# Performance work log

Hardware: AMD Instinct MI355X
Metric: run time of the kernel (lower is better)

The kernel has to match this reference:

```python
import jax, jax.numpy as jnp
import numpy as np

B, L, Z, H = 8, 256, 16, 256


def setup_inputs() -> dict:
    key = jax.random.key(0)
    k1, k2, k3, k4 = jax.random.split(key, 4)
    start_logits = jax.random.normal(k1, (B, L, H), dtype=jnp.float32)
    end_logits = jax.random.normal(k2, (B, L, H), dtype=jnp.float32)
    cls_logits = jax.random.normal(k3, (B, Z, H), dtype=jnp.float32)
    # nn.init.normal_(std=0.1)
    weight_start_end = 0.1 * jax.random.normal(k4, (H, H, H), dtype=jnp.float32)
    return {
        "start_logits": start_logits,
        "end_logits": end_logits,
        "cls_logits": cls_logits,
        "weight_start_end": weight_start_end,
    }


def reference(start_logits, end_logits, cls_logits, weight_start_end):
    # start: [b,x,i], weight: [i,o,j], end: [b,y,j], cls: [b,z,o]
    # Stage 1a: contract i ->  [b,x,o,j]  (GEMM: (b*x, i) @ (i, o*j))
    sw = jnp.einsum('bxi,ioj->bxoj', start_logits, weight_start_end)
    # Stage 1b: contract j ->  [b,x,y,o]
    start_end = jnp.einsum('bxoj,byj->bxyo', sw, end_logits)
    # Stage 2: contract o ->  [b,x,y,z]
    span_logits = jnp.einsum('bxyo,bzo->bxyz', start_end, cls_logits)
    return span_logits
```

## Files before the change

### kernel.cpp

```cpp
#include <hip/hip_runtime.h>
#include <hip/hip_bf16.h>


typedef __attribute__((ext_vector_type(8))) short      bf16x8;
typedef __attribute__((ext_vector_type(8))) unsigned short u16x8;
typedef __attribute__((ext_vector_type(4))) float      f32x4;

#define LDST 40

__device__ __forceinline__ unsigned short f2bf(float f) {
    unsigned u = __builtin_bit_cast(unsigned, f);
    u += 0x7fff + ((u >> 16) & 1);
    return (unsigned short)(u >> 16);
}

template<bool AB16, bool BB16, bool BTRANS, bool CB16>
__global__ __launch_bounds__(256)
void gemm_mfma(const void* __restrict__ Abv, const void* __restrict__ Bbv,
               void* __restrict__ Cbv,
               int lda, int ldb, int ldc,
               long aBS, int aSh, long bBS, int bSh, long cBS)
{
    __shared__ unsigned short As[128 * LDST];
    __shared__ unsigned short Bs[128 * LDST];

    const int tid  = threadIdx.x;
    const int bz   = blockIdx.z;
    const int row0 = blockIdx.y * 128;
    const int col0 = blockIdx.x * 128;

    const float*          Af = (const float*)Abv          + (long)(bz >> aSh) * aBS;
    const unsigned short* Ah = (const unsigned short*)Abv + (long)(bz >> aSh) * aBS;
    const float*          Bf = (const float*)Bbv          + (long)(bz >> bSh) * bBS;
    const unsigned short* Bh = (const unsigned short*)Bbv + (long)(bz >> bSh) * bBS;
    float*          Cf = (float*)Cbv          + (long)bz * cBS;
    unsigned short* Ch = (unsigned short*)Cbv + (long)bz * cBS;

    const int ar  = tid >> 2;
    const int akc = tid & 3;
    const int bk2 = (tid & 15) * 2;
    const int bn0 = (tid >> 4) * 8;

    const int wid = tid >> 6, lane = tid & 63;
    const int wm = wid >> 1, wn = wid & 1;
    const int lr = lane & 15, lg = lane >> 4;

    f32x4 acc[4][4] = {};

    float4 aPf[2][2]; u16x8 aPh[2];
    float4 bNf[2][2]; u16x8 bNh[2];
    float4 bTf[4];    u16x8 bTh[2];

    auto LOAD = [&](int k0) {
#pragma unroll
        for (int it = 0; it < 2; ++it) {
            if constexpr (!AB16) {
                const float* p = Af + (long)(row0 + ar + 64 * it) * lda + k0 + akc * 8;
                aPf[it][0] = *(const float4*)p;
                aPf[it][1] = *(const float4*)(p + 4);
            } else {
                aPh[it] = *(const u16x8*)(Ah + (long)(row0 + ar + 64 * it) * lda + k0 + akc * 8);
            }
            if constexpr (!BTRANS) {
                if constexpr (!BB16) {
                    const float* p = Bf + (long)(col0 + ar + 64 * it) * ldb + k0 + akc * 8;
                    bNf[it][0] = *(const float4*)p;
                    bNf[it][1] = *(const float4*)(p + 4);
                } else {
                    bNh[it] = *(const u16x8*)(Bh + (long)(col0 + ar + 64 * it) * ldb + k0 + akc * 8);
                }
            }
        }
        if constexpr (BTRANS) {
            if constexpr (!BB16) {
                const float* p = Bf + (long)(k0 + bk2) * ldb + col0 + bn0;
                bTf[0] = *(const float4*)p;
                bTf[1] = *(const float4*)(p + 4);
                bTf[2] = *(const float4*)(p + ldb);
                bTf[3] = *(const float4*)(p + ldb + 4);
            } else {
                const unsigned short* p = Bh + (long)(k0 + bk2) * ldb + col0 + bn0;
                bTh[0] = *(const u16x8*)p;
                bTh[1] = *(const u16x8*)(p + ldb);
            }
        }
    };

    auto WRITE = [&]() {
#pragma unroll
        for (int it = 0; it < 2; ++it) {
            u16x8 w;
            if constexpr (!AB16) {
                const float* v = (const float*)&aPf[it][0];
#pragma unroll
                for (int e = 0; e < 8; ++e) w[e] = f2bf(v[e]);
            } else {
                w = aPh[it];
            }
            *(u16x8*)(As + (ar + 64 * it) * LDST + akc * 8) = w;

            if constexpr (!BTRANS) {
                u16x8 wb;
                if constexpr (!BB16) {
                    const float* v = (const float*)&bNf[it][0];
#pragma unroll
                    for (int e = 0; e < 8; ++e) wb[e] = f2bf(v[e]);
                } else {
                    wb = bNh[it];
                }
                *(u16x8*)(Bs + (ar + 64 * it) * LDST + akc * 8) = wb;
            }
        }
        if constexpr (BTRANS) {
#pragma unroll
            for (int e = 0; e < 8; ++e) {
                unsigned lo, hi;
                if constexpr (!BB16) {
                    const float* v0 = (const float*)&bTf[0];
                    const float* v1 = (const float*)&bTf[2];
                    lo = f2bf(v0[e]); hi = f2bf(v1[e]);
                } else {
                    lo = bTh[0][e]; hi = bTh[1][e];
                }
                *(unsigned*)(Bs + (bn0 + e) * LDST + bk2) = lo | (hi << 16);
            }
        }
    };

    auto COMPUTE = [&]() {
        bf16x8 aF[4], bF[4];
#pragma unroll
        for (int f = 0; f < 4; ++f) {
            aF[f] = *(const bf16x8*)&As[(wm * 64 + f * 16 + lr) * LDST + lg * 8];
            bF[f] = *(const bf16x8*)&Bs[(wn * 64 + f * 16 + lr) * LDST + lg * 8];
        }
#pragma unroll
        for (int fm = 0; fm < 4; ++fm)
#pragma unroll
            for (int fn = 0; fn < 4; ++fn)
                acc[fm][fn] = __builtin_amdgcn_mfma_f32_16x16x32_bf16(
                    aF[fm], bF[fn], acc[fm][fn], 0, 0, 0);
    };

    LOAD(0);
#pragma unroll
    for (int s = 0; s < 8; ++s) {
        WRITE();
        if (s < 7) LOAD((s + 1) * 32);
        __syncthreads();
        COMPUTE();
        __syncthreads();
    }

#pragma unroll
    for (int fm = 0; fm < 4; ++fm)
#pragma unroll
        for (int q = 0; q < 4; ++q) {
            const long row = row0 + wm * 64 + fm * 16 + lg * 4 + q;
#pragma unroll
            for (int fn = 0; fn < 4; ++fn) {
                const int col = col0 + wn * 64 + fn * 16 + lr;
                if constexpr (CB16) Ch[row * ldc + col] = f2bf(acc[fm][fn][q]);
                else                Cf[row * ldc + col] = acc[fm][fn][q];
            }
        }
}

__global__ __launch_bounds__(256)
void ztranspose(const float* __restrict__ tmp, float* __restrict__ out)
{
    __shared__ float lds[256][17];
    const int tid = threadIdx.x;
    const int b = blockIdx.x >> 8;
    const int x = blockIdx.x & 255;

#pragma unroll
    for (int z = 0; z < 16; ++z)
        lds[tid][z] = tmp[((long)(b * 16 + z) * 256 + x) * 256 + tid];
    __syncthreads();

    float* op = out + (long)(b * 256 + x) * 4096;
#pragma unroll
    for (int q = 0; q < 4; ++q) {
        const int y  = q * 64 + (tid >> 2);
        const int z0 = (tid & 3) * 4;
        float4 v = { lds[y][z0], lds[y][z0 + 1], lds[y][z0 + 2], lds[y][z0 + 3] };
        *(float4*)(op + (q * 256 + tid) * 4) = v;
    }
}

extern "C" void kernel_launch(void* const* d_in, const int* in_sizes, int n_in,
                              void* d_out, int out_size, void* d_ws, size_t ws_size,
                              hipStream_t stream)
{
    const float* start = (const float*)d_in[0];
    const float* endl  = (const float*)d_in[1];
    const float* cls   = (const float*)d_in[2];
    const float* W     = (const float*)d_in[3];
    float* out = (float*)d_out;

    unsigned short* Wc  = (unsigned short*)d_ws;
    unsigned short* T   = (unsigned short*)d_out;
    float*          tmp = (float*)d_ws;

    hipLaunchKernelGGL((gemm_mfma<false, false, true, true>), dim3(2, 1, 256), dim3(256), 0, stream,
        (const void*)cls, (const void*)W, (void*)Wc,
        256, 256, 65536, 0L, 0, 65536L, 0, 256L);

    hipLaunchKernelGGL((gemm_mfma<false, true, true, true>), dim3(2, 2, 128), dim3(256), 0, stream,
        (const void*)start, (const void*)Wc, (void*)T,
        256, 256, 256, 65536L, 4, 65536L, 0, 65536L);

    hipLaunchKernelGGL((gemm_mfma<true, false, false, false>), dim3(2, 2, 128), dim3(256), 0, stream,
        (const void*)T, (const void*)endl, (void*)tmp,
        256, 256, 256, 65536L, 0, 65536L, 4, 65536L);

    hipLaunchKernelGGL(ztranspose, dim3(2048), dim3(256), 0, stream, tmp, out);
}
```

Baseline: 157.3 us.

## Double-buffer LDS tiles, use 512-thread blocks, and vectorize transpose loads

The GEMM kernel moves to 512 threads per block, so each wave computes a 32x64 sub-tile. LDS tiles are now double-buffered, which drops one barrier per k-step and lets global-to-LDS writes for the next stage overlap the MFMA work on the current buffer. MFMA sections are raised in priority with s_setprio. The z-transpose kernel now reads float4 vectors instead of scalars. The trade-off is more LDS per block and a hand-written waitcnt/barrier sequence that has to stay correct for the buffer reuse.

```diff
diff --git a/kernel.cpp b/kernel.cpp
--- a/kernel.cpp
+++ b/kernel.cpp
@@ -1,10 +1,10 @@
 #include <hip/hip_runtime.h>
-#include <hip/hip_bf16.h>
-
-
-typedef __attribute__((ext_vector_type(8))) short      bf16x8;
+
+
+typedef __attribute__((ext_vector_type(8))) short          bf16x8;
 typedef __attribute__((ext_vector_type(8))) unsigned short u16x8;
-typedef __attribute__((ext_vector_type(4))) float      f32x4;
+typedef __attribute__((ext_vector_type(4))) unsigned short u16x4;
+typedef __attribute__((ext_vector_type(4))) float          f32x4;
 
 #define LDST 40
 
@@ -15,14 +15,14 @@
 }
 
 template<bool AB16, bool BB16, bool BTRANS, bool CB16>
-__global__ __launch_bounds__(256)
+__global__ __launch_bounds__(512, 4)
 void gemm_mfma(const void* __restrict__ Abv, const void* __restrict__ Bbv,
                void* __restrict__ Cbv,
                int lda, int ldb, int ldc,
                long aBS, int aSh, long bBS, int bSh, long cBS)
 {
-    __shared__ unsigned short As[128 * LDST];
-    __shared__ unsigned short Bs[128 * LDST];
+    __shared__ unsigned short As[2][128 * LDST];
+    __shared__ unsigned short Bs[2][128 * LDST];
 
     const int tid  = threadIdx.x;
     const int bz   = blockIdx.z;
@@ -38,125 +38,119 @@
 
     const int ar  = tid >> 2;
     const int akc = tid & 3;
-    const int bk2 = (tid & 15) * 2;
-    const int bn0 = (tid >> 4) * 8;
+    const int kp  = (tid >> 5) * 2;
+    const int ng  = (tid & 31) * 4;
 
     const int wid = tid >> 6, lane = tid & 63;
     const int wm = wid >> 1, wn = wid & 1;
     const int lr = lane & 15, lg = lane >> 4;
 
-    f32x4 acc[4][4] = {};
-
-    float4 aPf[2][2]; u16x8 aPh[2];
-    float4 bNf[2][2]; u16x8 bNh[2];
-    float4 bTf[4];    u16x8 bTh[2];
+    f32x4 acc[2][4] = {};
+
+    float4 aPf[2]; u16x8 aPh;
+    float4 bNf[2]; u16x8 bNh;
+    float4 bTf[2]; u16x4 bTh[2];
 
     auto LOAD = [&](int k0) {
-#pragma unroll
-        for (int it = 0; it < 2; ++it) {
-            if constexpr (!AB16) {
-                const float* p = Af + (long)(row0 + ar + 64 * it) * lda + k0 + akc * 8;
-                aPf[it][0] = *(const float4*)p;
-                aPf[it][1] = *(const float4*)(p + 4);
+        if constexpr (!AB16) {
+            const float* p = Af + (long)(row0 + ar) * lda + k0 + akc * 8;
+            aPf[0] = *(const float4*)p;
+            aPf[1] = *(const float4*)(p + 4);
+        } else {
+            aPh = *(const u16x8*)(Ah + (long)(row0 + ar) * lda + k0 + akc * 8);
+        }
+        if constexpr (!BTRANS) {
+            if constexpr (!BB16) {
+                const float* p = Bf + (long)(col0 + ar) * ldb + k0 + akc * 8;
+                bNf[0] = *(const float4*)p;
+                bNf[1] = *(const float4*)(p + 4);
             } else {
-                aPh[it] = *(const u16x8*)(Ah + (long)(row0 + ar + 64 * it) * lda + k0 + akc * 8);
-            }
-            if constexpr (!BTRANS) {
-                if constexpr (!BB16) {
-                    const float* p = Bf + (long)(col0 + ar + 64 * it) * ldb + k0 + akc * 8;
-                    bNf[it][0] = *(const float4*)p;
-                    bNf[it][1] = *(const float4*)(p + 4);
-                } else {
-                    bNh[it] = *(const u16x8*)(Bh + (long)(col0 + ar + 64 * it) * ldb + k0 + akc * 8);
-                }
-            }
-        }
-        if constexpr (BTRANS) {
+                bNh = *(const u16x8*)(Bh + (long)(col0 + ar) * ldb + k0 + akc * 8);
+            }
+        } else {
             if constexpr (!BB16) {
-                const float* p = Bf + (long)(k0 + bk2) * ldb + col0 + bn0;
+                const float* p = Bf + (long)(k0 + kp) * ldb + col0 + ng;
                 bTf[0] = *(const float4*)p;
-                bTf[1] = *(const float4*)(p + 4);
-                bTf[2] = *(const float4*)(p + ldb);
-                bTf[3] = *(const float4*)(p + ldb + 4);
+                bTf[1] = *(const float4*)(p + ldb);
             } else {
-                const unsigned short* p = Bh + (long)(k0 + bk2) * ldb + col0 + bn0;
-                bTh[0] = *(const u16x8*)p;
-                bTh[1] = *(const u16x8*)(p + ldb);
+                const unsigned short* p = Bh + (long)(k0 + kp) * ldb + col0 + ng;
+                bTh[0] = *(const u16x4*)p;
+                bTh[1] = *(const u16x4*)(p + ldb);
             }
         }
     };
 
-    auto WRITE = [&]() {
-#pragma unroll
-        for (int it = 0; it < 2; ++it) {
-            u16x8 w;
-            if constexpr (!AB16) {
-                const float* v = (const float*)&aPf[it][0];
-#pragma unroll
-                for (int e = 0; e < 8; ++e) w[e] = f2bf(v[e]);
+    auto WRITE = [&](int buf) {
+        u16x8 w;
+        if constexpr (!AB16) {
+            const float* v = (const float*)&aPf[0];
+#pragma unroll
+            for (int e = 0; e < 8; ++e) w[e] = f2bf(v[e]);
+        } else {
+            w = aPh;
+        }
+        *(u16x8*)(As[buf] + ar * LDST + akc * 8) = w;
+
+        if constexpr (!BTRANS) {
+            u16x8 wb;
+            if constexpr (!BB16) {
+                const float* v = (const float*)&bNf[0];
+#pragma unroll
+                for (int e = 0; e < 8; ++e) wb[e] = f2bf(v[e]);
             } else {
-                w = aPh[it];
-            }
-            *(u16x8*)(As + (ar + 64 * it) * LDST + akc * 8) = w;
-
-            if constexpr (!BTRANS) {
-                u16x8 wb;
-                if constexpr (!BB16) {
-                    const float* v = (const float*)&bNf[it][0];
-#pragma unroll
-                    for (int e = 0; e < 8; ++e) wb[e] = f2bf(v[e]);
-                } else {
-                    wb = bNh[it];
-                }
-                *(u16x8*)(Bs + (ar + 64 * it) * LDST + akc * 8) = wb;
-            }
-        }
-        if constexpr (BTRANS) {
-#pragma unroll
-            for (int e = 0; e < 8; ++e) {
+                wb = bNh;
+            }
+            *(u16x8*)(Bs[buf] + ar * LDST + akc * 8) = wb;
+        } else {
+#pragma unroll
+            for (int e = 0; e < 4; ++e) {
                 unsigned lo, hi;
                 if constexpr (!BB16) {
                     const float* v0 = (const float*)&bTf[0];
-                    const float* v1 = (const float*)&bTf[2];
+                    const float* v1 = (const float*)&bTf[1];
                     lo = f2bf(v0[e]); hi = f2bf(v1[e]);
                 } else {
                     lo = bTh[0][e]; hi = bTh[1][e];
                 }
-                *(unsigned*)(Bs + (bn0 + e) * LDST + bk2) = lo | (hi << 16);
+                *(unsigned*)(Bs[buf] + (ng + e) * LDST + kp) = lo | (hi << 16);
             }
         }
     };
 
-    auto COMPUTE = [&]() {
-        bf16x8 aF[4], bF[4];
-#pragma unroll
-        for (int f = 0; f < 4; ++f) {
-            aF[f] = *(const bf16x8*)&As[(wm * 64 + f * 16 + lr) * LDST + lg * 8];
-            bF[f] = *(const bf16x8*)&Bs[(wn * 64 + f * 16 + lr) * LDST + lg * 8];
-        }
-#pragma unroll
-        for (int fm = 0; fm < 4; ++fm)
+    auto COMPUTE = [&](int buf) {
+        bf16x8 aF[2], bF[4];
+#pragma unroll
+        for (int fm = 0; fm < 2; ++fm)
+            aF[fm] = *(const bf16x8*)&As[buf][(wm * 32 + fm * 16 + lr) * LDST + lg * 8];
+#pragma unroll
+        for (int fn = 0; fn < 4; ++fn)
+            bF[fn] = *(const bf16x8*)&Bs[buf][(wn * 64 + fn * 16 + lr) * LDST + lg * 8];
+        __builtin_amdgcn_s_setprio(1);
+#pragma unroll
+        for (int fm = 0; fm < 2; ++fm)
 #pragma unroll
             for (int fn = 0; fn < 4; ++fn)
                 acc[fm][fn] = __builtin_amdgcn_mfma_f32_16x16x32_bf16(
                     aF[fm], bF[fn], acc[fm][fn], 0, 0, 0);
+        __builtin_amdgcn_s_setprio(0);
     };
 
     LOAD(0);
+    WRITE(0);
 #pragma unroll
     for (int s = 0; s < 8; ++s) {
-        WRITE();
         if (s < 7) LOAD((s + 1) * 32);
-        __syncthreads();
-        COMPUTE();
-        __syncthreads();
+        asm volatile("s_waitcnt lgkmcnt(0)" ::: "memory");
+        __builtin_amdgcn_s_barrier();
+        COMPUTE(s & 1);
+        if (s < 7) WRITE((s + 1) & 1);
     }
 
 #pragma unroll
-    for (int fm = 0; fm < 4; ++fm)
+    for (int fm = 0; fm < 2; ++fm)
 #pragma unroll
         for (int q = 0; q < 4; ++q) {
-            const long row = row0 + wm * 64 + fm * 16 + lg * 4 + q;
+            const long row = row0 + wm * 32 + fm * 16 + lg * 4 + q;
 #pragma unroll
             for (int fn = 0; fn < 4; ++fn) {
                 const int col = col0 + wn * 64 + fn * 16 + lr;
@@ -173,10 +167,17 @@
     const int tid = threadIdx.x;
     const int b = blockIdx.x >> 8;
     const int x = blockIdx.x & 255;
-
-#pragma unroll
-    for (int z = 0; z < 16; ++z)
-        lds[tid][z] = tmp[((long)(b * 16 + z) * 256 + x) * 256 + tid];
+    const int w = tid >> 6, l = tid & 63;
+
+#pragma unroll
+    for (int rep = 0; rep < 4; ++rep) {
+        const int z = rep * 4 + w;
+        float4 v = *(const float4*)(tmp + ((long)(b * 16 + z) * 256 + x) * 256 + l * 4);
+        lds[l * 4 + 0][z] = v.x;
+        lds[l * 4 + 1][z] = v.y;
+        lds[l * 4 + 2][z] = v.z;
+        lds[l * 4 + 3][z] = v.w;
+    }
     __syncthreads();
 
     float* op = out + (long)(b * 256 + x) * 4096;
@@ -203,15 +204,15 @@
     unsigned short* T   = (unsigned short*)d_out;
     float*          tmp = (float*)d_ws;
 
-    hipLaunchKernelGGL((gemm_mfma<false, false, true, true>), dim3(2, 1, 256), dim3(256), 0, stream,
+    hipLaunchKernelGGL((gemm_mfma<false, false, true, true>), dim3(2, 1, 256), dim3(512), 0, stream,
         (const void*)cls, (const void*)W, (void*)Wc,
         256, 256, 65536, 0L, 0, 65536L, 0, 256L);
 
-    hipLaunchKernelGGL((gemm_mfma<false, true, true, true>), dim3(2, 2, 128), dim3(256), 0, stream,
+    hipLaunchKernelGGL((gemm_mfma<false, true, true, true>), dim3(2, 2, 128), dim3(512), 0, stream,
         (const void*)start, (const void*)Wc, (void*)T,
         256, 256, 256, 65536L, 4, 65536L, 0, 65536L);
 
-    hipLaunchKernelGGL((gemm_mfma<true, false, false, false>), dim3(2, 2, 128), dim3(256), 0, stream,
+    hipLaunchKernelGGL((gemm_mfma<true, false, false, false>), dim3(2, 2, 128), dim3(512), 0, stream,
         (const void*)T, (const void*)endl, (void*)tmp,
         256, 256, 256, 65536L, 0, 65536L, 4, 65536L);
 
```

Result: no change. 158.1 us (+0.5%).
